# Optimization experiments

Measured on AMD Instinct MI355X. Metric: run time of the kernel, lower is better.

## Reference

```python
import jax, jax.numpy as jnp
import numpy as np

BM = 64; BN = 64          # block_m, block_n
NKM = BM // 4; NKN = BN // 4   # tokens sampled per block (16)
# topk_newtype bands: cumulative-pooled-attention fraction -> granularity value (0 = skip block)
RATIO_BANDS = [(1, 0.05), (2, 0.15), (4, 0.25), (8, 0.5)]


def setup_inputs() -> dict:
    key = jax.random.key(0)
    kq, kk, kv, ki, kj = jax.random.split(key, 5)
    B, H, L, D = 1, 8, 4096, 64
    q = jax.random.normal(kq, (B, H, L, D), jnp.float32)
    k = jax.random.normal(kk, (B, H, L, D), jnp.float32)
    v = jax.random.normal(kv, (B, H, L, D), jnp.float32)
    # distinct in-block sample positions, shared across blocks per (B,H)
    # (mirrors torch.topk(torch.rand(B,H,1,block), sample_num))
    sample_idx_q = jnp.argsort(jax.random.uniform(ki, (B, H, BM)), axis=-1)[..., :NKM].astype(jnp.int32)
    sample_idx_k = jnp.argsort(jax.random.uniform(kj, (B, H, BN)), axis=-1)[..., :NKN].astype(jnp.int32)
    return {"q": q, "k": k, "v": v, "sample_idx_q": sample_idx_q, "sample_idx_k": sample_idx_k}


def _sample_blocks(x, idx, bs, nk):
    # x: [B,H,L,D]; idx: [B,H,nk] in-block positions -> [B,H,nb*nk,D]
    B, H, L, D = x.shape
    nb = L // bs
    xb = x.reshape(B, H, nb, bs, D)
    gidx = jnp.broadcast_to(idx[:, :, None, :, None], (B, H, nb, nk, D))
    return jnp.take_along_axis(xb, gidx, axis=3).reshape(B, H, nb * nk, D)


def _block_mask(q, k, sample_idx_q, sample_idx_k):
    # pooled downsampled attention -> per-(q_block,k_block) keep mask (topk_newtype)
    B, H, L, D = q.shape
    qb, kb = L // BM, L // BN
    sq = _sample_blocks(q, sample_idx_q, BM, NKM)  # [B,H,qb*NKM,D]
    sk = _sample_blocks(k, sample_idx_k, BN, NKN)  # [B,H,kb*NKN,D]
    scores = jnp.einsum('bhqd,bhkd->bhqk', sq, sk) / jnp.sqrt(jnp.float32(D))
    attn = jax.nn.softmax(scores, axis=-1)
    # NKM x NKN sum-pooling == block-level pooled attention mass  [B,H,qb,kb]
    pooling = attn.reshape(B, H, qb, NKM, kb, NKN).sum(axis=(3, 5))
    # rank key-blocks per q-block row by pooled mass, band by cumulative fraction
    order = jnp.argsort(-pooling, axis=-1)
    sp = jnp.take_along_axis(pooling, order, axis=-1)
    cs = jnp.cumsum(sp, axis=-1)
    frac_before = (cs - sp) / cs[..., -1:]
    val = jnp.zeros_like(sp)
    for g, hi in RATIO_BANDS[::-1]:
        val = jnp.where(frac_before < hi, jnp.float32(g), val)
    rank = jnp.argsort(order, axis=-1)          # inverse permutation
    mask_vals = jnp.take_along_axis(val, rank, axis=-1)  # [B,H,qb,kb] in {0,1,2,4,8}
    return mask_vals > 0


def reference(q, k, v, sample_idx_q, sample_idx_k):
    B, H, L, D = q.shape
    attend = _block_mask(q, k, sample_idx_q, sample_idx_k)            # [B,H,qb,kb]
    attend_tok = jnp.repeat(jnp.repeat(attend, BM, axis=2), BN, axis=3)  # [B,H,L,L]
    scores = jnp.einsum('bhqd,bhkd->bhqk', q, k) / jnp.sqrt(jnp.float32(D))
    scores = jnp.where(attend_tok, scores, jnp.float32(-1e30))
    p = jax.nn.softmax(scores, axis=-1)
    return jnp.einsum('bhqk,bhkd->bhqd', p, v)
```

## Files before the change

kernel.cpp:

```cpp
#include <hip/hip_runtime.h>
#include <hip/hip_bf16.h>

#define H_ 8
#define L_ 4096
#define D_ 64
#define NB_ 64

typedef __attribute__((ext_vector_type(8))) short bf16x8;
typedef __attribute__((ext_vector_type(4))) float f32x4;

__device__ __forceinline__ unsigned short f2bf(float x) {
    unsigned u = __float_as_uint(x);
    u += 0x7fff + ((u >> 16) & 1);
    return (unsigned short)(u >> 16);
}
__device__ __forceinline__ float bf2f(unsigned short s) {
    return __uint_as_float(((unsigned)s) << 16);
}
__device__ __forceinline__ void gload_lds16(const unsigned short* g, unsigned short* l) {
    __builtin_amdgcn_global_load_lds(
        (const __attribute__((address_space(1))) unsigned int*)(const void*)g,
        (__attribute__((address_space(3))) unsigned int*)(void*)l,
        16, 0, 0);
}

__global__ __launch_bounds__(256) void prep_kernel(
    const float* __restrict__ q, const float* __restrict__ k, const float* __restrict__ v,
    const int* __restrict__ sidxk,
    unsigned short* __restrict__ qhi, unsigned short* __restrict__ qlo,
    unsigned short* __restrict__ khi,
    unsigned short* __restrict__ vth,
    unsigned short* __restrict__ skh, unsigned short* __restrict__ skl)
{
    const int h  = blockIdx.x >> 6;
    const int tb = blockIdx.x & 63;
    const int tid = threadIdx.x;
    __shared__ float vst[64][68];

    const size_t te = ((size_t)(h*64 + tb)) << 12;
    const float4* qg = (const float4*)(q + te);
    for (int i4 = tid; i4 < 1024; i4 += 256) {
        float4 t = qg[i4];
        ushort4 hi, lo;
        hi.x = f2bf(t.x); lo.x = f2bf(t.x - bf2f(hi.x));
        hi.y = f2bf(t.y); lo.y = f2bf(t.y - bf2f(hi.y));
        hi.z = f2bf(t.z); lo.z = f2bf(t.z - bf2f(hi.z));
        hi.w = f2bf(t.w); lo.w = f2bf(t.w - bf2f(hi.w));
        *(ushort4*)(qhi + te + i4*4) = hi;
        *(ushort4*)(qlo + te + i4*4) = lo;
    }
    const float4* kg = (const float4*)(k + te);
    for (int i4 = tid; i4 < 1024; i4 += 256) {
        float4 t = kg[i4];
        int r = i4 >> 4, c4 = i4 & 15;
        int sch = (c4 >> 1) ^ ((r >> 2) & 7);
        ushort4 hi;
        hi.x = f2bf(t.x); hi.y = f2bf(t.y); hi.z = f2bf(t.z); hi.w = f2bf(t.w);
        *(ushort4*)(khi + te + r*64 + sch*8 + (c4 & 1)*4) = hi;
    }
    {
        int t = tid >> 4, d4 = tid & 15;
        int srow = tb*64 + sidxk[h*16 + t];
        float4 x = *(const float4*)(k + ((size_t)h*L_ + srow)*D_ + d4*4);
        ushort4 hi, lo;
        hi.x = f2bf(x.x); lo.x = f2bf(x.x - bf2f(hi.x));
        hi.y = f2bf(x.y); lo.y = f2bf(x.y - bf2f(hi.y));
        hi.z = f2bf(x.z); lo.z = f2bf(x.z - bf2f(hi.z));
        hi.w = f2bf(x.w); lo.w = f2bf(x.w - bf2f(hi.w));
        int sch = (d4 >> 1) ^ (t & 7);
        size_t dst = ((size_t)h*1024 + tb*16 + t)*64 + sch*8 + (d4 & 1)*4;
        *(ushort4*)(skh + dst) = hi;
        *(ushort4*)(skl + dst) = lo;
    }
    const float4* vg = (const float4*)(v + te);
    for (int i4 = tid; i4 < 1024; i4 += 256) {
        float4 t = vg[i4];
        *(float4*)&vst[i4 >> 4][(i4 & 15)*4] = t;
    }
    __syncthreads();
    for (int u = tid; u < 512; u += 256) {
        int d = u >> 3, kc8 = u & 7;
        int sch = kc8 ^ (d & 7);
        ushort4 h0, h1;
        h0.x = f2bf(vst[kc8*8+0][d]); h0.y = f2bf(vst[kc8*8+1][d]);
        h0.z = f2bf(vst[kc8*8+2][d]); h0.w = f2bf(vst[kc8*8+3][d]);
        h1.x = f2bf(vst[kc8*8+4][d]); h1.y = f2bf(vst[kc8*8+5][d]);
        h1.z = f2bf(vst[kc8*8+6][d]); h1.w = f2bf(vst[kc8*8+7][d]);
        *(ushort4*)(vth + te + d*64 + sch*8 + 0) = h0;
        *(ushort4*)(vth + te + d*64 + sch*8 + 4) = h1;
    }
}

__global__ __launch_bounds__(256, 4) void mask_mfma(
    const unsigned short* __restrict__ qhi, const unsigned short* __restrict__ qlo,
    const unsigned short* __restrict__ skh, const unsigned short* __restrict__ skl,
    const int* __restrict__ sidxq,
    unsigned long long* __restrict__ maskbits)
{
    const int h    = blockIdx.x & 7;
    const int qb   = blockIdx.x >> 3;
    const int tid  = threadIdx.x;
    const int wave = tid >> 6;
    const int lane = tid & 63;
    const int l16  = lane & 15;
    const int quad = lane >> 4;

    __shared__ __align__(16) unsigned short ch[8192];
    __shared__ __align__(16) unsigned short cl[8192];
    __shared__ float E[16][64];
    __shared__ float Z[16];
    __shared__ float pooled[64];

    for (int e = tid; e < 16*64; e += 256) (&E[0][0])[e] = 0.f;

    const int iqr = sidxq[h*16 + l16];
    const size_t qo = (((size_t)(h*64 + qb)) << 12) + (size_t)iqr*64;
    bf16x8 qh[2], ql[2];
    qh[0] = *(const bf16x8*)(qhi + qo + quad*8);
    qh[1] = *(const bf16x8*)(qhi + qo + 32 + quad*8);
    ql[0] = *(const bf16x8*)(qlo + qo + quad*8);
    ql[1] = *(const bf16x8*)(qlo + qo + 32 + quad*8);
    __syncthreads();

    for (int cc = 0; cc < 8; ++cc) {
        const bf16x8* gh = (const bf16x8*)(skh + ((size_t)h*1024 + cc*128)*64);
        const bf16x8* gl = (const bf16x8*)(skl + ((size_t)h*1024 + cc*128)*64);
        for (int i = tid; i < 1024; i += 256) {
            ((bf16x8*)ch)[i] = gh[i];
            ((bf16x8*)cl)[i] = gl[i];
        }
        __syncthreads();

        #pragma unroll
        for (int tt = 0; tt < 2; ++tt) {
            const int kb = cc*8 + wave*2 + tt;
            const int nb = (wave*2 + tt)*16;
            f32x4 sacc = (f32x4){0.f, 0.f, 0.f, 0.f};
            #pragma unroll
            for (int kc = 0; kc < 2; ++kc) {
                const int off = (nb + l16)*64 + (((kc*4 + quad) ^ (l16 & 7))*8);
                bf16x8 kh = *(const bf16x8*)&ch[off];
                bf16x8 kl = *(const bf16x8*)&cl[off];
                sacc = __builtin_amdgcn_mfma_f32_16x16x32_bf16(qh[kc], kh, sacc, 0, 0, 0);
                sacc = __builtin_amdgcn_mfma_f32_16x16x32_bf16(qh[kc], kl, sacc, 0, 0, 0);
                sacc = __builtin_amdgcn_mfma_f32_16x16x32_bf16(ql[kc], kh, sacc, 0, 0, 0);
                sacc = __builtin_amdgcn_mfma_f32_16x16x32_bf16(ql[kc], kl, sacc, 0, 0, 0);
            }
            #pragma unroll
            for (int r = 0; r < 4; ++r) {
                float p = __expf(sacc[r] * 0.125f);
                p += __shfl_xor(p, 1);
                p += __shfl_xor(p, 2);
                p += __shfl_xor(p, 4);
                p += __shfl_xor(p, 8);
                if (l16 == 0) E[quad*4 + r][kb] = p;
            }
        }
        __syncthreads();
    }

    if (tid < 16) {
        float s = 0.f;
        #pragma unroll
        for (int kb = 0; kb < 64; ++kb) s += E[tid][kb];
        Z[tid] = s;
    }
    __syncthreads();
    if (tid < 64) {
        float s = 0.f;
        #pragma unroll
        for (int t = 0; t < 16; ++t) s += E[t][tid] / Z[t];
        pooled[tid] = s;
    }
    __syncthreads();
    if (tid < 64) {
        float pi = pooled[tid];
        float tot = 0.f, bef = 0.f;
        for (int j2 = 0; j2 < 64; ++j2) {
            float pj = pooled[j2];
            tot += pj;
            if (pj > pi || (pj == pi && j2 < tid)) bef += pj;
        }
        bool att = (bef / tot) < 0.5f;
        unsigned long long bits = __ballot(att);
        if (tid == 0) maskbits[h*64 + qb] = bits;
    }
}

__global__ __launch_bounds__(256, 2) void attn_fast(
    const unsigned short* __restrict__ qhi, const unsigned short* __restrict__ qlo,
    const unsigned short* __restrict__ khi,
    const unsigned short* __restrict__ vth,
    const unsigned long long* __restrict__ maskbits,
    float* __restrict__ out)
{
    const int h    = blockIdx.x & 7;
    const int qb   = blockIdx.x >> 3;
    const int tid  = threadIdx.x;
    const int wave = tid >> 6;
    const int lane = tid & 63;
    const int l16  = lane & 15;
    const int quad = lane >> 4;

    __shared__ __align__(16) unsigned short bufK[2][4096];
    __shared__ __align__(16) unsigned short bufVh[2][4096];
    __shared__ __align__(16) unsigned short ps[4][16][88];

    const size_t qoff = (((size_t)(h*64 + qb)) << 12) + (size_t)(wave*16 + l16)*64;
    bf16x8 qfh[2], qfl[2];
    qfh[0] = *(const bf16x8*)(qhi + qoff + quad*8);
    qfh[1] = *(const bf16x8*)(qhi + qoff + 32 + quad*8);
    qfl[0] = *(const bf16x8*)(qlo + qoff + quad*8);
    qfl[1] = *(const bf16x8*)(qlo + qoff + 32 + quad*8);

    const unsigned long long bm = maskbits[(h << 6) + qb];

    float lpart[4];
    f32x4 oacc[4];
    #pragma unroll
    for (int r = 0; r < 4; ++r) lpart[r] = 0.f;
    #pragma unroll
    for (int t = 0; t < 4; ++t) oacc[t] = (f32x4){0.f, 0.f, 0.f, 0.f};

    auto dma_stage = [&](int kb, int b) {
        const size_t tb = ((size_t)(h*64 + kb)) << 12;
        gload_lds16(khi + tb + tid*8,         &bufK [b][tid*8]);
        gload_lds16(khi + tb + (tid+256)*8,   &bufK [b][(tid+256)*8]);
        gload_lds16(vth + tb + tid*8,         &bufVh[b][tid*8]);
        gload_lds16(vth + tb + (tid+256)*8,   &bufVh[b][(tid+256)*8]);
    };

    auto compute = [&](int b) {
        f32x4 sacc[4];
        #pragma unroll
        for (int t = 0; t < 4; ++t) sacc[t] = (f32x4){0.f, 0.f, 0.f, 0.f};
        #pragma unroll
        for (int t = 0; t < 4; ++t) {
            #pragma unroll
            for (int kc = 0; kc < 2; ++kc) {
                bf16x8 kf = *(const bf16x8*)&bufK[b][(l16*4 + t)*64 + (((kc*4 + quad) ^ (l16 & 7))*8)];
                sacc[t] = __builtin_amdgcn_mfma_f32_16x16x32_bf16(qfh[kc], kf, sacc[t], 0, 0, 0);
                sacc[t] = __builtin_amdgcn_mfma_f32_16x16x32_bf16(qfl[kc], kf, sacc[t], 0, 0, 0);
            }
        }
        #pragma unroll
        for (int r = 0; r < 4; ++r) {
            float p0 = __expf(fmaf(sacc[0][r], 0.125f, -16.0f));
            float p1 = __expf(fmaf(sacc[1][r], 0.125f, -16.0f));
            float p2 = __expf(fmaf(sacc[2][r], 0.125f, -16.0f));
            float p3 = __expf(fmaf(sacc[3][r], 0.125f, -16.0f));
            __hip_bfloat162 a01 = __float22bfloat162_rn(make_float2(p0, p1));
            __hip_bfloat162 a23 = __float22bfloat162_rn(make_float2(p2, p3));
            unsigned u01 = *(unsigned*)&a01;
            unsigned u23 = *(unsigned*)&a23;
            uint2 w; w.x = u01; w.y = u23;
            *(uint2*)&ps[wave][quad*4 + r][l16*4] = w;
            lpart[r] += (bf2f((unsigned short)(u01 & 0xffffu)) + bf2f((unsigned short)(u01 >> 16)))
                      + (bf2f((unsigned short)(u23 & 0xffffu)) + bf2f((unsigned short)(u23 >> 16)));
        }
        bf16x8 pf[2];
        #pragma unroll
        for (int kc = 0; kc < 2; ++kc)
            pf[kc] = *(const bf16x8*)&ps[wave][l16][kc*32 + quad*8];
        #pragma unroll
        for (int t = 0; t < 4; ++t) {
            #pragma unroll
            for (int kc = 0; kc < 2; ++kc) {
                bf16x8 vh = *(const bf16x8*)&bufVh[b][(t*16 + l16)*64 + (((kc*4 + quad) ^ (l16 & 7))*8)];
                oacc[t] = __builtin_amdgcn_mfma_f32_16x16x32_bf16(pf[kc], vh, oacc[t], 0, 0, 0);
            }
        }
    };

    unsigned long long rem = bm;
    int cur = 0;
    {
        int kb0 = (int)__builtin_ctzll(rem); rem &= rem - 1;
        dma_stage(kb0, 0);
    }
    for (;;) {
        __syncthreads();
        int nxt = -1;
        if (rem) { nxt = (int)__builtin_ctzll(rem); rem &= rem - 1; dma_stage(nxt, cur ^ 1); }
        compute(cur);
        if (nxt < 0) break;
        cur ^= 1;
    }

    #pragma unroll
    for (int off = 1; off < 16; off <<= 1)
        #pragma unroll
        for (int r = 0; r < 4; ++r)
            lpart[r] += __shfl_xor(lpart[r], off);

    float* og = out + ((size_t)h*L_ + (size_t)qb*64)*D_ + (size_t)(wave*16 + quad*4)*D_;
    #pragma unroll
    for (int r = 0; r < 4; ++r) {
        float inv = 1.f / lpart[r];
        #pragma unroll
        for (int t = 0; t < 4; ++t)
            og[(size_t)r*D_ + t*16 + l16] = oacc[t][r] * inv;
    }
}

__global__ __launch_bounds__(256, 4) void mask_kernel4(
    const float* __restrict__ q, const float* __restrict__ k,
    const int* __restrict__ sidxq, const int* __restrict__ sidxk,
    unsigned long long* __restrict__ maskbits)
{
    const int h   = blockIdx.x >> 6;
    const int qb  = blockIdx.x & 63;
    const int tid = threadIdx.x;
    const int rg  = tid >> 5;
    const int cg  = tid & 31;

    __shared__ float sq[16][68];
    __shared__ float skc[128][68];
    __shared__ float E[16][64];
    __shared__ float Z[16];
    __shared__ float pooled[64];
    __shared__ int iq[16], ik[16];

    if (tid < 16) { iq[tid] = sidxq[h*16 + tid]; ik[tid] = sidxk[h*16 + tid]; }
    for (int e = tid; e < 16*64; e += 256) (&E[0][0])[e] = 0.f;
    __syncthreads();
    {
        int j = tid >> 4, d4 = tid & 15;
        int grow = h*L_ + qb*64 + iq[j];
        *(float4*)&sq[j][d4*4] = *(const float4*)(q + (size_t)grow*D_ + d4*4);
    }
    for (int cc = 0; cc < 8; ++cc) {
        for (int i = tid; i < 2048; i += 256) {
            int col = i >> 4, d4 = i & 15;
            int colg = cc*128 + col;
            int grow = h*L_ + (colg >> 4)*64 + ik[colg & 15];
            *(float4*)&skc[col][d4*4] = *(const float4*)(k + (size_t)grow*D_ + d4*4);
        }
        __syncthreads();
        float acc[2][4] = {{0.f,0.f,0.f,0.f},{0.f,0.f,0.f,0.f}};
        #pragma unroll 4
        for (int d4 = 0; d4 < 16; ++d4) {
            float4 qv0 = *(const float4*)&sq[rg*2 + 0][d4*4];
            float4 qv1 = *(const float4*)&sq[rg*2 + 1][d4*4];
            #pragma unroll
            for (int j = 0; j < 4; ++j) {
                float4 kv = *(const float4*)&skc[cg + 32*j][d4*4];
                acc[0][j] += qv0.x*kv.x + qv0.y*kv.y + qv0.z*kv.z + qv0.w*kv.w;
                acc[1][j] += qv1.x*kv.x + qv1.y*kv.y + qv1.z*kv.z + qv1.w*kv.w;
            }
        }
        #pragma unroll
        for (int j = 0; j < 4; ++j) {
            int kb = cc*8 + (cg >> 4) + 2*j;
            #pragma unroll
            for (int i = 0; i < 2; ++i) {
                float p = __expf(acc[i][j] * 0.125f);
                p += __shfl_xor(p, 1);
                p += __shfl_xor(p, 2);
                p += __shfl_xor(p, 4);
                p += __shfl_xor(p, 8);
                if ((cg & 15) == 0) E[rg*2 + i][kb] += p;
            }
        }
        __syncthreads();
    }
    if (tid < 16) {
        float s = 0.f;
        #pragma unroll
        for (int kb = 0; kb < 64; ++kb) s += E[tid][kb];
        Z[tid] = s;
    }
    __syncthreads();
    if (tid < 64) {
        float s = 0.f;
        #pragma unroll
        for (int t = 0; t < 16; ++t) s += E[t][tid] / Z[t];
        pooled[tid] = s;
    }
    __syncthreads();
    if (tid < 64) {
        float pi = pooled[tid];
        float tot = 0.f, bef = 0.f;
        for (int j2 = 0; j2 < 64; ++j2) {
            float pj = pooled[j2];
            tot += pj;
            if (pj > pi || (pj == pi && j2 < tid)) bef += pj;
        }
        bool att = (bef / tot) < 0.5f;
        unsigned long long bits = __ballot(att);
        if (tid == 0) maskbits[h*64 + qb] = bits;
    }
}

__global__ __launch_bounds__(256, 3) void attn_v3(
    const float* __restrict__ q, const float* __restrict__ k, const float* __restrict__ v,
    const unsigned long long* __restrict__ maskbits, float* __restrict__ out)
{
    const int h = blockIdx.x >> 6, qb = blockIdx.x & 63;
    const int tid = threadIdx.x, wave = tid >> 6, lane = tid & 63;
    const int l16 = lane & 15, quad = lane >> 4;
    __shared__ __align__(16) unsigned short ks_hi[64][72];
    __shared__ __align__(16) unsigned short ks_lo[64][72];
    __shared__ __align__(16) unsigned short vt_hi[64][72];
    __shared__ __align__(16) unsigned short vt_lo[64][72];
    __shared__ __align__(16) unsigned short ps[4][16][72];

    const float4* qg = (const float4*)(q + ((size_t)h*L_ + (size_t)qb*64)*D_);
    for (int i4 = tid; i4 < 1024; i4 += 256) {
        float4 t = qg[i4];
        int r = i4 >> 4, c = (i4 & 15) << 2;
        ushort4 hi, lo;
        hi.x = f2bf(t.x); lo.x = f2bf(t.x - bf2f(hi.x));
        hi.y = f2bf(t.y); lo.y = f2bf(t.y - bf2f(hi.y));
        hi.z = f2bf(t.z); lo.z = f2bf(t.z - bf2f(hi.z));
        hi.w = f2bf(t.w); lo.w = f2bf(t.w - bf2f(hi.w));
        *(ushort4*)&ks_hi[r][c] = hi;
        *(ushort4*)&ks_lo[r][c] = lo;
    }
    const unsigned long long bm = maskbits[(h << 6) + qb];
    __syncthreads();
    bf16x8 qhi2[2], qlo2[2];
    #pragma unroll
    for (int kc = 0; kc < 2; ++kc) {
        qhi2[kc] = *(const bf16x8*)&ks_hi[wave*16 + l16][kc*32 + quad*8];
        qlo2[kc] = *(const bf16x8*)&ks_lo[wave*16 + l16][kc*32 + quad*8];
    }
    __syncthreads();
    float m_i[4], l_i[4];
    f32x4 oacc[4];
    #pragma unroll
    for (int r = 0; r < 4; ++r) { m_i[r] = -1e30f; l_i[r] = 0.f; }
    #pragma unroll
    for (int t = 0; t < 4; ++t) oacc[t] = (f32x4){0.f, 0.f, 0.f, 0.f};
    for (int kb = 0; kb < 64; ++kb) {
        if (!((bm >> kb) & 1ull)) continue;
        const float4* kg = (const float4*)(k + ((size_t)h*L_ + (size_t)kb*64)*D_);
        const float*  vg = v + ((size_t)h*L_ + (size_t)kb*64)*D_;
        for (int i4 = tid; i4 < 1024; i4 += 256) {
            float4 t = kg[i4];
            int r = i4 >> 4, c = (i4 & 15) << 2;
            ushort4 hi, lo;
            hi.x = f2bf(t.x); lo.x = f2bf(t.x - bf2f(hi.x));
            hi.y = f2bf(t.y); lo.y = f2bf(t.y - bf2f(hi.y));
            hi.z = f2bf(t.z); lo.z = f2bf(t.z - bf2f(hi.z));
            hi.w = f2bf(t.w); lo.w = f2bf(t.w - bf2f(hi.w));
            *(ushort4*)&ks_hi[r][c] = hi;
            *(ushort4*)&ks_lo[r][c] = lo;
        }
        for (int tsk = tid; tsk < 512; tsk += 256) {
            int rp = tsk >> 4;
            int c  = (tsk & 15) << 2;
            float4 a0 = *(const float4*)(vg + (size_t)(2*rp)*D_ + c);
            float4 a1 = *(const float4*)(vg + (size_t)(2*rp+1)*D_ + c);
            #pragma unroll
            for (int j = 0; j < 4; ++j) {
                float x0 = (j==0)?a0.x:(j==1)?a0.y:(j==2)?a0.z:a0.w;
                float x1 = (j==0)?a1.x:(j==1)?a1.y:(j==2)?a1.z:a1.w;
                unsigned short h0 = f2bf(x0), h1b = f2bf(x1);
                *(unsigned*)&vt_hi[c+j][2*rp] = (unsigned)h0 | ((unsigned)h1b << 16);
                unsigned short lo0 = f2bf(x0 - bf2f(h0)), lo1 = f2bf(x1 - bf2f(h1b));
                *(unsigned*)&vt_lo[c+j][2*rp] = (unsigned)lo0 | ((unsigned)lo1 << 16);
            }
        }
        __syncthreads();
        f32x4 sacc[4];
        #pragma unroll
        for (int t = 0; t < 4; ++t) sacc[t] = (f32x4){0.f, 0.f, 0.f, 0.f};
        #pragma unroll
        for (int t = 0; t < 4; ++t) {
            #pragma unroll
            for (int kc = 0; kc < 2; ++kc) {
                bf16x8 khi2 = *(const bf16x8*)&ks_hi[t*16 + l16][kc*32 + quad*8];
                bf16x8 klo2 = *(const bf16x8*)&ks_lo[t*16 + l16][kc*32 + quad*8];
                sacc[t] = __builtin_amdgcn_mfma_f32_16x16x32_bf16(qhi2[kc], khi2, sacc[t], 0, 0, 0);
                sacc[t] = __builtin_amdgcn_mfma_f32_16x16x32_bf16(qhi2[kc], klo2, sacc[t], 0, 0, 0);
                sacc[t] = __builtin_amdgcn_mfma_f32_16x16x32_bf16(qlo2[kc], khi2, sacc[t], 0, 0, 0);
            }
        }
        #pragma unroll
        for (int t = 0; t < 4; ++t) sacc[t] *= 0.125f;
        float rowmax[4];
        #pragma unroll
        for (int r = 0; r < 4; ++r)
            rowmax[r] = fmaxf(fmaxf(sacc[0][r], sacc[1][r]), fmaxf(sacc[2][r], sacc[3][r]));
        #pragma unroll
        for (int off = 1; off < 16; off <<= 1)
            #pragma unroll
            for (int r = 0; r < 4; ++r)
                rowmax[r] = fmaxf(rowmax[r], __shfl_xor(rowmax[r], off));
        float al[4], rs[4];
        #pragma unroll
        for (int r = 0; r < 4; ++r) {
            float mnew = fmaxf(m_i[r], rowmax[r]);
            al[r] = __expf(m_i[r] - mnew);
            m_i[r] = mnew;
            float acc = 0.f;
            #pragma unroll
            for (int t = 0; t < 4; ++t) {
                float p = __expf(sacc[t][r] - mnew);
                unsigned short pb = f2bf(p);
                ps[wave][quad*4 + r][t*16 + l16] = pb;
                acc += bf2f(pb);
            }
            rs[r] = acc;
        }
        #pragma unroll
        for (int off = 1; off < 16; off <<= 1)
            #pragma unroll
            for (int r = 0; r < 4; ++r)
                rs[r] += __shfl_xor(rs[r], off);
        #pragma unroll
        for (int r = 0; r < 4; ++r) l_i[r] = l_i[r] * al[r] + rs[r];
        #pragma unroll
        for (int t = 0; t < 4; ++t)
            #pragma unroll
            for (int r = 0; r < 4; ++r) oacc[t][r] *= al[r];
        bf16x8 pf[2];
        #pragma unroll
        for (int kc = 0; kc < 2; ++kc)
            pf[kc] = *(const bf16x8*)&ps[wave][l16][kc*32 + quad*8];
        #pragma unroll
        for (int t = 0; t < 4; ++t) {
            #pragma unroll
            for (int kc = 0; kc < 2; ++kc) {
                bf16x8 vhif = *(const bf16x8*)&vt_hi[t*16 + l16][kc*32 + quad*8];
                bf16x8 vlof = *(const bf16x8*)&vt_lo[t*16 + l16][kc*32 + quad*8];
                oacc[t] = __builtin_amdgcn_mfma_f32_16x16x32_bf16(pf[kc], vhif, oacc[t], 0, 0, 0);
                oacc[t] = __builtin_amdgcn_mfma_f32_16x16x32_bf16(pf[kc], vlof, oacc[t], 0, 0, 0);
            }
        }
        __syncthreads();
    }
    float* og = out + ((size_t)h*L_ + (size_t)qb*64)*D_ + (size_t)(wave*16 + quad*4)*D_;
    #pragma unroll
    for (int r = 0; r < 4; ++r) {
        float inv = 1.f / l_i[r];
        #pragma unroll
        for (int t = 0; t < 4; ++t)
            og[(size_t)r*D_ + t*16 + l16] = oacc[t][r] * inv;
    }
}

extern "C" void kernel_launch(void* const* d_in, const int* in_sizes, int n_in,
                              void* d_out, int out_size, void* d_ws, size_t ws_size,
                              hipStream_t stream) {
    const float* q = (const float*)d_in[0];
    const float* k = (const float*)d_in[1];
    const float* v = (const float*)d_in[2];
    const int* siq = (const int*)d_in[3];
    const int* sik = (const int*)d_in[4];
    float* out = (float*)d_out;

    char* ws = (char*)d_ws;
    unsigned long long* mask = (unsigned long long*)ws;
    const size_t TEN = (size_t)H_*L_*D_;
    const size_t SKN = (size_t)H_*1024*64;
    unsigned short* qhi = (unsigned short*)(ws + 4096);
    unsigned short* qlo = qhi + TEN;
    unsigned short* khi = qlo + TEN;
    unsigned short* vth = khi + TEN;
    unsigned short* skh = vth + TEN;
    unsigned short* skl = skh + SKN;
    const size_t need = 4096 + (4*TEN + 2*SKN)*sizeof(unsigned short);

    if (ws_size >= need) {
        prep_kernel<<<dim3(H_*NB_), dim3(256), 0, stream>>>(q, k, v, sik, qhi, qlo, khi, vth, skh, skl);
        mask_mfma<<<dim3(H_*NB_), dim3(256), 0, stream>>>(qhi, qlo, skh, skl, siq, mask);
        attn_fast<<<dim3(H_*NB_), dim3(256), 0, stream>>>(qhi, qlo, khi, vth, mask, out);
    } else {
        mask_kernel4<<<dim3(H_*NB_), dim3(256), 0, stream>>>(q, k, siq, sik, mask);
        attn_v3<<<dim3(H_*NB_), dim3(256), 0, stream>>>(q, k, v, mask, out);
    }
}
```

Baseline: 146.7 us.

## Triple-buffer K/V tiles with explicit vmcnt waits and MFMA priority boosts

The K/V LDS staging grows from two buffers to three, so two tiles are prefetched ahead and each iteration waits only for the oldest outstanding DMA (vmcnt(4)) instead of fully draining. The synchronisation becomes a raw s_barrier with a sched_barrier, and the MFMA sections are wrapped in s_setprio to favour matrix work over other waves. LDS use grows by 16 KB per block, which may limit the intended two blocks per CU. Correctness depends on the hand-counted vmcnt values and on the write-after-read ordering of the ring buffer.

```diff
diff --git a/kernel.cpp b/kernel.cpp
--- a/kernel.cpp
+++ b/kernel.cpp
@@ -202,8 +202,8 @@
     const int l16  = lane & 15;
     const int quad = lane >> 4;
 
-    __shared__ __align__(16) unsigned short bufK[2][4096];
-    __shared__ __align__(16) unsigned short bufVh[2][4096];
+    __shared__ __align__(16) unsigned short bufK [3][4096];
+    __shared__ __align__(16) unsigned short bufVh[3][4096];
     __shared__ __align__(16) unsigned short ps[4][16][88];
 
     const size_t qoff = (((size_t)(h*64 + qb)) << 12) + (size_t)(wave*16 + l16)*64;
@@ -234,6 +234,7 @@
         f32x4 sacc[4];
         #pragma unroll
         for (int t = 0; t < 4; ++t) sacc[t] = (f32x4){0.f, 0.f, 0.f, 0.f};
+        __builtin_amdgcn_s_setprio(1);
         #pragma unroll
         for (int t = 0; t < 4; ++t) {
             #pragma unroll
@@ -243,6 +244,7 @@
                 sacc[t] = __builtin_amdgcn_mfma_f32_16x16x32_bf16(qfl[kc], kf, sacc[t], 0, 0, 0);
             }
         }
+        __builtin_amdgcn_s_setprio(0);
         #pragma unroll
         for (int r = 0; r < 4; ++r) {
             float p0 = __expf(fmaf(sacc[0][r], 0.125f, -16.0f));
@@ -262,6 +264,7 @@
         #pragma unroll
         for (int kc = 0; kc < 2; ++kc)
             pf[kc] = *(const bf16x8*)&ps[wave][l16][kc*32 + quad*8];
+        __builtin_amdgcn_s_setprio(1);
         #pragma unroll
         for (int t = 0; t < 4; ++t) {
             #pragma unroll
@@ -270,21 +273,36 @@
                 oacc[t] = __builtin_amdgcn_mfma_f32_16x16x32_bf16(pf[kc], vh, oacc[t], 0, 0, 0);
             }
         }
+        __builtin_amdgcn_s_setprio(0);
     };
 
     unsigned long long rem = bm;
-    int cur = 0;
+    int cur = 0, have_nxt = 0;
     {
         int kb0 = (int)__builtin_ctzll(rem); rem &= rem - 1;
         dma_stage(kb0, 0);
+        if (rem) {
+            int kb1 = (int)__builtin_ctzll(rem); rem &= rem - 1;
+            dma_stage(kb1, 1);
+            have_nxt = 1;
+        }
     }
     for (;;) {
-        __syncthreads();
-        int nxt = -1;
-        if (rem) { nxt = (int)__builtin_ctzll(rem); rem &= rem - 1; dma_stage(nxt, cur ^ 1); }
+        if (have_nxt) { asm volatile("s_waitcnt vmcnt(4)" ::: "memory"); }
+        else          { asm volatile("s_waitcnt vmcnt(0)" ::: "memory"); }
+        __builtin_amdgcn_sched_barrier(0);
+        __builtin_amdgcn_s_barrier();
+        int nxt2 = 0;
+        if (have_nxt && rem) {
+            int kb2 = (int)__builtin_ctzll(rem); rem &= rem - 1;
+            int b2 = cur + 2; if (b2 >= 3) b2 -= 3;
+            dma_stage(kb2, b2);
+            nxt2 = 1;
+        }
         compute(cur);
-        if (nxt < 0) break;
-        cur ^= 1;
+        if (!have_nxt) break;
+        have_nxt = nxt2;
+        cur = cur + 1; if (cur >= 3) cur = 0;
     }
 
     #pragma unroll
```

Result: faster. 143.8 us (-2.0%).

## Split attention key blocks across two workgroups and combine partial sums

Applied to the files above, without the earlier changes.

The attention kernel now launches two workgroups per (head, q-block), each taking alternating key blocks from the mask. The two write unnormalised partial outputs and row sums, and a new combine kernel adds and normalises them. The change aims to raise parallelism and occupancy on a 512-block grid with few active key blocks. It also splits the K and V staging so V has a single buffer with explicit waitcnt and barriers, and raises MFMA priority with setprio. In exchange it adds an extra kernel launch and a round trip of partial results through global memory.

```diff
diff --git a/kernel.cpp b/kernel.cpp
--- a/kernel.cpp
+++ b/kernel.cpp
@@ -187,15 +187,16 @@
     }
 }
 
-__global__ __launch_bounds__(256, 2) void attn_fast(
+__global__ __launch_bounds__(256, 4) void attn_split(
     const unsigned short* __restrict__ qhi, const unsigned short* __restrict__ qlo,
     const unsigned short* __restrict__ khi,
     const unsigned short* __restrict__ vth,
     const unsigned long long* __restrict__ maskbits,
-    float* __restrict__ out)
+    float* __restrict__ part_o, float* __restrict__ part_l)
 {
-    const int h    = blockIdx.x & 7;
-    const int qb   = blockIdx.x >> 3;
+    const int h     = blockIdx.x & 7;
+    const int qb    = (blockIdx.x >> 3) & 63;
+    const int split = blockIdx.x >> 9;
     const int tid  = threadIdx.x;
     const int wave = tid >> 6;
     const int lane = tid & 63;
@@ -203,7 +204,7 @@
     const int quad = lane >> 4;
 
     __shared__ __align__(16) unsigned short bufK[2][4096];
-    __shared__ __align__(16) unsigned short bufVh[2][4096];
+    __shared__ __align__(16) unsigned short bufV[4096];
     __shared__ __align__(16) unsigned short ps[4][16][88];
 
     const size_t qoff = (((size_t)(h*64 + qb)) << 12) + (size_t)(wave*16 + l16)*64;
@@ -213,7 +214,8 @@
     qfl[0] = *(const bf16x8*)(qlo + qoff + quad*8);
     qfl[1] = *(const bf16x8*)(qlo + qoff + 32 + quad*8);
 
-    const unsigned long long bm = maskbits[(h << 6) + qb];
+    unsigned long long rem = maskbits[(h << 6) + qb];
+    if (split && rem) rem &= rem - 1;
 
     float lpart[4];
     f32x4 oacc[4];
@@ -222,69 +224,83 @@
     #pragma unroll
     for (int t = 0; t < 4; ++t) oacc[t] = (f32x4){0.f, 0.f, 0.f, 0.f};
 
-    auto dma_stage = [&](int kb, int b) {
+    auto stage_K = [&](int kb, int b) {
         const size_t tb = ((size_t)(h*64 + kb)) << 12;
-        gload_lds16(khi + tb + tid*8,         &bufK [b][tid*8]);
-        gload_lds16(khi + tb + (tid+256)*8,   &bufK [b][(tid+256)*8]);
-        gload_lds16(vth + tb + tid*8,         &bufVh[b][tid*8]);
-        gload_lds16(vth + tb + (tid+256)*8,   &bufVh[b][(tid+256)*8]);
+        gload_lds16(khi + tb + tid*8,       &bufK[b][tid*8]);
+        gload_lds16(khi + tb + (tid+256)*8, &bufK[b][(tid+256)*8]);
     };
-
-    auto compute = [&](int b) {
-        f32x4 sacc[4];
-        #pragma unroll
-        for (int t = 0; t < 4; ++t) sacc[t] = (f32x4){0.f, 0.f, 0.f, 0.f};
-        #pragma unroll
-        for (int t = 0; t < 4; ++t) {
-            #pragma unroll
-            for (int kc = 0; kc < 2; ++kc) {
-                bf16x8 kf = *(const bf16x8*)&bufK[b][(l16*4 + t)*64 + (((kc*4 + quad) ^ (l16 & 7))*8)];
-                sacc[t] = __builtin_amdgcn_mfma_f32_16x16x32_bf16(qfh[kc], kf, sacc[t], 0, 0, 0);
-                sacc[t] = __builtin_amdgcn_mfma_f32_16x16x32_bf16(qfl[kc], kf, sacc[t], 0, 0, 0);
-            }
-        }
-        #pragma unroll
-        for (int r = 0; r < 4; ++r) {
-            float p0 = __expf(fmaf(sacc[0][r], 0.125f, -16.0f));
-            float p1 = __expf(fmaf(sacc[1][r], 0.125f, -16.0f));
-            float p2 = __expf(fmaf(sacc[2][r], 0.125f, -16.0f));
-            float p3 = __expf(fmaf(sacc[3][r], 0.125f, -16.0f));
-            __hip_bfloat162 a01 = __float22bfloat162_rn(make_float2(p0, p1));
-            __hip_bfloat162 a23 = __float22bfloat162_rn(make_float2(p2, p3));
-            unsigned u01 = *(unsigned*)&a01;
-            unsigned u23 = *(unsigned*)&a23;
-            uint2 w; w.x = u01; w.y = u23;
-            *(uint2*)&ps[wave][quad*4 + r][l16*4] = w;
-            lpart[r] += (bf2f((unsigned short)(u01 & 0xffffu)) + bf2f((unsigned short)(u01 >> 16)))
-                      + (bf2f((unsigned short)(u23 & 0xffffu)) + bf2f((unsigned short)(u23 >> 16)));
-        }
-        bf16x8 pf[2];
-        #pragma unroll
-        for (int kc = 0; kc < 2; ++kc)
-            pf[kc] = *(const bf16x8*)&ps[wave][l16][kc*32 + quad*8];
-        #pragma unroll
-        for (int t = 0; t < 4; ++t) {
-            #pragma unroll
-            for (int kc = 0; kc < 2; ++kc) {
-                bf16x8 vh = *(const bf16x8*)&bufVh[b][(t*16 + l16)*64 + (((kc*4 + quad) ^ (l16 & 7))*8)];
-                oacc[t] = __builtin_amdgcn_mfma_f32_16x16x32_bf16(pf[kc], vh, oacc[t], 0, 0, 0);
-            }
-        }
+    auto stage_V = [&](int kb) {
+        const size_t tb = ((size_t)(h*64 + kb)) << 12;
+        gload_lds16(vth + tb + tid*8,       &bufV[tid*8]);
+        gload_lds16(vth + tb + (tid+256)*8, &bufV[(tid+256)*8]);
     };
 
-    unsigned long long rem = bm;
-    int cur = 0;
-    {
-        int kb0 = (int)__builtin_ctzll(rem); rem &= rem - 1;
-        dma_stage(kb0, 0);
-    }
-    for (;;) {
-        __syncthreads();
-        int nxt = -1;
-        if (rem) { nxt = (int)__builtin_ctzll(rem); rem &= rem - 1; dma_stage(nxt, cur ^ 1); }
-        compute(cur);
-        if (nxt < 0) break;
-        cur ^= 1;
+    if (rem) {
+        int kb_cur = (int)__builtin_ctzll(rem);
+        rem &= rem - 1; if (rem) rem &= rem - 1;
+        stage_K(kb_cur, 0);
+        int cur = 0;
+        for (;;) {
+            asm volatile("s_waitcnt vmcnt(0)" ::: "memory");
+            __builtin_amdgcn_sched_barrier(0);
+            __builtin_amdgcn_s_barrier();
+            stage_V(kb_cur);
+            int kb_nxt = -1;
+            if (rem) {
+                kb_nxt = (int)__builtin_ctzll(rem);
+                rem &= rem - 1; if (rem) rem &= rem - 1;
+                stage_K(kb_nxt, cur ^ 1);
+            }
+            f32x4 sacc[4];
+            #pragma unroll
+            for (int t = 0; t < 4; ++t) sacc[t] = (f32x4){0.f, 0.f, 0.f, 0.f};
+            __builtin_amdgcn_s_setprio(1);
+            #pragma unroll
+            for (int t = 0; t < 4; ++t) {
+                #pragma unroll
+                for (int kc = 0; kc < 2; ++kc) {
+                    bf16x8 kf = *(const bf16x8*)&bufK[cur][(l16*4 + t)*64 + (((kc*4 + quad) ^ (l16 & 7))*8)];
+                    sacc[t] = __builtin_amdgcn_mfma_f32_16x16x32_bf16(qfh[kc], kf, sacc[t], 0, 0, 0);
+                    sacc[t] = __builtin_amdgcn_mfma_f32_16x16x32_bf16(qfl[kc], kf, sacc[t], 0, 0, 0);
+                }
+            }
+            __builtin_amdgcn_s_setprio(0);
+            #pragma unroll
+            for (int r = 0; r < 4; ++r) {
+                float p0 = __expf(fmaf(sacc[0][r], 0.125f, -16.0f));
+                float p1 = __expf(fmaf(sacc[1][r], 0.125f, -16.0f));
+                float p2 = __expf(fmaf(sacc[2][r], 0.125f, -16.0f));
+                float p3 = __expf(fmaf(sacc[3][r], 0.125f, -16.0f));
+                __hip_bfloat162 a01 = __float22bfloat162_rn(make_float2(p0, p1));
+                __hip_bfloat162 a23 = __float22bfloat162_rn(make_float2(p2, p3));
+                unsigned u01 = *(unsigned*)&a01;
+                unsigned u23 = *(unsigned*)&a23;
+                uint2 w; w.x = u01; w.y = u23;
+                *(uint2*)&ps[wave][quad*4 + r][l16*4] = w;
+                lpart[r] += (bf2f((unsigned short)(u01 & 0xffffu)) + bf2f((unsigned short)(u01 >> 16)))
+                          + (bf2f((unsigned short)(u23 & 0xffffu)) + bf2f((unsigned short)(u23 >> 16)));
+            }
+            if (kb_nxt >= 0) { asm volatile("s_waitcnt vmcnt(2)" ::: "memory"); }
+            else             { asm volatile("s_waitcnt vmcnt(0)" ::: "memory"); }
+            __builtin_amdgcn_sched_barrier(0);
+            __builtin_amdgcn_s_barrier();
+            bf16x8 pf[2];
+            #pragma unroll
+            for (int kc = 0; kc < 2; ++kc)
+                pf[kc] = *(const bf16x8*)&ps[wave][l16][kc*32 + quad*8];
+            __builtin_amdgcn_s_setprio(1);
+            #pragma unroll
+            for (int t = 0; t < 4; ++t) {
+                #pragma unroll
+                for (int kc = 0; kc < 2; ++kc) {
+                    bf16x8 vh = *(const bf16x8*)&bufV[(t*16 + l16)*64 + (((kc*4 + quad) ^ (l16 & 7))*8)];
+                    oacc[t] = __builtin_amdgcn_mfma_f32_16x16x32_bf16(pf[kc], vh, oacc[t], 0, 0, 0);
+                }
+            }
+            __builtin_amdgcn_s_setprio(0);
+            if (kb_nxt < 0) break;
+            kb_cur = kb_nxt; cur ^= 1;
+        }
     }
 
     #pragma unroll
@@ -293,13 +309,42 @@
         for (int r = 0; r < 4; ++r)
             lpart[r] += __shfl_xor(lpart[r], off);
 
-    float* og = out + ((size_t)h*L_ + (size_t)qb*64)*D_ + (size_t)(wave*16 + quad*4)*D_;
-    #pragma unroll
-    for (int r = 0; r < 4; ++r) {
-        float inv = 1.f / lpart[r];
+    const size_t blk = (size_t)split*512 + (size_t)(h*64 + qb);
+    float* po = part_o + (blk*64 + (size_t)(wave*16 + quad*4))*64;
+    #pragma unroll
+    for (int r = 0; r < 4; ++r)
         #pragma unroll
         for (int t = 0; t < 4; ++t)
-            og[(size_t)r*D_ + t*16 + l16] = oacc[t][r] * inv;
+            po[(size_t)r*64 + t*16 + l16] = oacc[t][r];
+    if (l16 == 0) {
+        #pragma unroll
+        for (int r = 0; r < 4; ++r)
+            part_l[blk*64 + wave*16 + quad*4 + r] = lpart[r];
+    }
+}
+
+__global__ __launch_bounds__(256) void combine_kernel(
+    const float* __restrict__ part_o, const float* __restrict__ part_l,
+    float* __restrict__ out)
+{
+    const int hq  = blockIdx.x;
+    const int tid = threadIdx.x;
+    const int row = tid >> 2;
+    const int d0  = (tid & 3) << 4;
+    const size_t S1o = (size_t)512*64*64;
+    const float l = part_l[(size_t)hq*64 + row] + part_l[(size_t)512*64 + hq*64 + row];
+    const float inv = 1.f / l;
+    const size_t base = ((size_t)hq*64 + row)*64 + d0;
+    #pragma unroll
+    for (int j = 0; j < 16; j += 4) {
+        float4 a = *(const float4*)(part_o + base + j);
+        float4 b = *(const float4*)(part_o + S1o + base + j);
+        float4 r;
+        r.x = (a.x + b.x) * inv;
+        r.y = (a.y + b.y) * inv;
+        r.z = (a.z + b.z) * inv;
+        r.w = (a.w + b.w) * inv;
+        *(float4*)(out + base + j) = r;
     }
 }
 
@@ -561,12 +606,16 @@
     unsigned short* vth = khi + TEN;
     unsigned short* skh = vth + TEN;
     unsigned short* skl = skh + SKN;
-    const size_t need = 4096 + (4*TEN + 2*SKN)*sizeof(unsigned short);
+    const size_t base_need = 4096 + (4*TEN + 2*SKN)*sizeof(unsigned short);
+    float* part_o = (float*)(ws + base_need);
+    float* part_l = part_o + (size_t)2*512*64*64;
+    const size_t need = base_need + ((size_t)2*512*64*64 + (size_t)2*512*64)*sizeof(float);
 
     if (ws_size >= need) {
         prep_kernel<<<dim3(H_*NB_), dim3(256), 0, stream>>>(q, k, v, sik, qhi, qlo, khi, vth, skh, skl);
         mask_mfma<<<dim3(H_*NB_), dim3(256), 0, stream>>>(qhi, qlo, skh, skl, siq, mask);
-        attn_fast<<<dim3(H_*NB_), dim3(256), 0, stream>>>(qhi, qlo, khi, vth, mask, out);
+        attn_split<<<dim3(H_*NB_*2), dim3(256), 0, stream>>>(qhi, qlo, khi, vth, mask, part_o, part_l);
+        combine_kernel<<<dim3(H_*NB_), dim3(256), 0, stream>>>(part_o, part_l, out);
     } else {
         mask_kernel4<<<dim3(H_*NB_), dim3(256), 0, stream>>>(q, k, siq, sik, mask);
         attn_v3<<<dim3(H_*NB_), dim3(256), 0, stream>>>(q, k, v, mask, out);
```

Result: no change. 148.6 us (+1.3%).

## Process key blocks in pairs with split K/V staging and explicit waitcnt pipelining

Applied to the files above, without the earlier changes.

The attention kernel now handles two selected key blocks per iteration. K tiles are double-buffered a step ahead, and V tiles are loaded separately, overlapping with the QK/softmax phase. Waits on outstanding loads use explicit vmcnt counts and raw barriers, MFMA sections are given higher scheduling priority, and exp is computed via exp2 with prescaled constants. This halves the number of barrier-bound iterations and hides V load latency, at the cost of more LDS (larger K buffer and P scratch) and tricky manual wait counts.

```diff
diff --git a/kernel.cpp b/kernel.cpp
--- a/kernel.cpp
+++ b/kernel.cpp
@@ -187,7 +187,7 @@
     }
 }
 
-__global__ __launch_bounds__(256, 2) void attn_fast(
+__global__ __launch_bounds__(256, 2) void attn_pair(
     const unsigned short* __restrict__ qhi, const unsigned short* __restrict__ qlo,
     const unsigned short* __restrict__ khi,
     const unsigned short* __restrict__ vth,
@@ -202,9 +202,9 @@
     const int l16  = lane & 15;
     const int quad = lane >> 4;
 
-    __shared__ __align__(16) unsigned short bufK[2][4096];
-    __shared__ __align__(16) unsigned short bufVh[2][4096];
-    __shared__ __align__(16) unsigned short ps[4][16][88];
+    __shared__ __align__(16) unsigned short bufK[2][2][4096];
+    __shared__ __align__(16) unsigned short bufV[2][4096];
+    __shared__ __align__(16) unsigned short ps[4][16][152];
 
     const size_t qoff = (((size_t)(h*64 + qb)) << 12) + (size_t)(wave*16 + l16)*64;
     bf16x8 qfh[2], qfl[2];
@@ -213,7 +213,7 @@
     qfl[0] = *(const bf16x8*)(qlo + qoff + quad*8);
     qfl[1] = *(const bf16x8*)(qlo + qoff + 32 + quad*8);
 
-    const unsigned long long bm = maskbits[(h << 6) + qb];
+    unsigned long long rem = maskbits[(h << 6) + qb];
 
     float lpart[4];
     f32x4 oacc[4];
@@ -222,69 +222,109 @@
     #pragma unroll
     for (int t = 0; t < 4; ++t) oacc[t] = (f32x4){0.f, 0.f, 0.f, 0.f};
 
-    auto dma_stage = [&](int kb, int b) {
+    auto stage_K1 = [&](int kb, int slot, int ta) {
         const size_t tb = ((size_t)(h*64 + kb)) << 12;
-        gload_lds16(khi + tb + tid*8,         &bufK [b][tid*8]);
-        gload_lds16(khi + tb + (tid+256)*8,   &bufK [b][(tid+256)*8]);
-        gload_lds16(vth + tb + tid*8,         &bufVh[b][tid*8]);
-        gload_lds16(vth + tb + (tid+256)*8,   &bufVh[b][(tid+256)*8]);
+        gload_lds16(khi + tb + tid*8,       &bufK[slot][ta][tid*8]);
+        gload_lds16(khi + tb + (tid+256)*8, &bufK[slot][ta][(tid+256)*8]);
     };
-
-    auto compute = [&](int b) {
+    auto stage_V1 = [&](int kb, int ta) {
+        const size_t tb = ((size_t)(h*64 + kb)) << 12;
+        gload_lds16(vth + tb + tid*8,       &bufV[ta][tid*8]);
+        gload_lds16(vth + tb + (tid+256)*8, &bufV[ta][(tid+256)*8]);
+    };
+
+    auto qk_sm = [&](int cur, int ta) {
         f32x4 sacc[4];
         #pragma unroll
         for (int t = 0; t < 4; ++t) sacc[t] = (f32x4){0.f, 0.f, 0.f, 0.f};
+        __builtin_amdgcn_s_setprio(1);
         #pragma unroll
         for (int t = 0; t < 4; ++t) {
             #pragma unroll
             for (int kc = 0; kc < 2; ++kc) {
-                bf16x8 kf = *(const bf16x8*)&bufK[b][(l16*4 + t)*64 + (((kc*4 + quad) ^ (l16 & 7))*8)];
+                bf16x8 kf = *(const bf16x8*)&bufK[cur][ta][(l16*4 + t)*64 + (((kc*4 + quad) ^ (l16 & 7))*8)];
                 sacc[t] = __builtin_amdgcn_mfma_f32_16x16x32_bf16(qfh[kc], kf, sacc[t], 0, 0, 0);
                 sacc[t] = __builtin_amdgcn_mfma_f32_16x16x32_bf16(qfl[kc], kf, sacc[t], 0, 0, 0);
             }
         }
+        __builtin_amdgcn_s_setprio(0);
         #pragma unroll
         for (int r = 0; r < 4; ++r) {
-            float p0 = __expf(fmaf(sacc[0][r], 0.125f, -16.0f));
-            float p1 = __expf(fmaf(sacc[1][r], 0.125f, -16.0f));
-            float p2 = __expf(fmaf(sacc[2][r], 0.125f, -16.0f));
-            float p3 = __expf(fmaf(sacc[3][r], 0.125f, -16.0f));
+            float p0 = __builtin_amdgcn_exp2f(fmaf(sacc[0][r], 0.18033688f, -23.083121f));
+            float p1 = __builtin_amdgcn_exp2f(fmaf(sacc[1][r], 0.18033688f, -23.083121f));
+            float p2 = __builtin_amdgcn_exp2f(fmaf(sacc[2][r], 0.18033688f, -23.083121f));
+            float p3 = __builtin_amdgcn_exp2f(fmaf(sacc[3][r], 0.18033688f, -23.083121f));
             __hip_bfloat162 a01 = __float22bfloat162_rn(make_float2(p0, p1));
             __hip_bfloat162 a23 = __float22bfloat162_rn(make_float2(p2, p3));
             unsigned u01 = *(unsigned*)&a01;
             unsigned u23 = *(unsigned*)&a23;
             uint2 w; w.x = u01; w.y = u23;
-            *(uint2*)&ps[wave][quad*4 + r][l16*4] = w;
+            *(uint2*)&ps[wave][quad*4 + r][ta*64 + l16*4] = w;
             lpart[r] += (bf2f((unsigned short)(u01 & 0xffffu)) + bf2f((unsigned short)(u01 >> 16)))
                       + (bf2f((unsigned short)(u23 & 0xffffu)) + bf2f((unsigned short)(u23 >> 16)));
         }
-        bf16x8 pf[2];
-        #pragma unroll
-        for (int kc = 0; kc < 2; ++kc)
-            pf[kc] = *(const bf16x8*)&ps[wave][l16][kc*32 + quad*8];
-        #pragma unroll
-        for (int t = 0; t < 4; ++t) {
-            #pragma unroll
-            for (int kc = 0; kc < 2; ++kc) {
-                bf16x8 vh = *(const bf16x8*)&bufVh[b][(t*16 + l16)*64 + (((kc*4 + quad) ^ (l16 & 7))*8)];
-                oacc[t] = __builtin_amdgcn_mfma_f32_16x16x32_bf16(pf[kc], vh, oacc[t], 0, 0, 0);
-            }
-        }
     };
 
-    unsigned long long rem = bm;
-    int cur = 0;
-    {
-        int kb0 = (int)__builtin_ctzll(rem); rem &= rem - 1;
-        dma_stage(kb0, 0);
-    }
-    for (;;) {
-        __syncthreads();
-        int nxt = -1;
-        if (rem) { nxt = (int)__builtin_ctzll(rem); rem &= rem - 1; dma_stage(nxt, cur ^ 1); }
-        compute(cur);
-        if (nxt < 0) break;
-        cur ^= 1;
+    if (rem) {
+        int ka = (int)__builtin_ctzll(rem); rem &= rem - 1;
+        int kb2 = -1;
+        if (rem) { kb2 = (int)__builtin_ctzll(rem); rem &= rem - 1; }
+        stage_K1(ka, 0, 0);
+        if (kb2 >= 0) stage_K1(kb2, 0, 1);
+        int cur = 0;
+        for (;;) {
+            asm volatile("s_waitcnt vmcnt(0)" ::: "memory");
+            __builtin_amdgcn_sched_barrier(0);
+            __builtin_amdgcn_s_barrier();
+            stage_V1(ka, 0);
+            if (kb2 >= 0) stage_V1(kb2, 1);
+            int na = -1, nb = -1;
+            if (rem) {
+                na = (int)__builtin_ctzll(rem); rem &= rem - 1;
+                if (rem) { nb = (int)__builtin_ctzll(rem); rem &= rem - 1; }
+                stage_K1(na, cur ^ 1, 0);
+                if (nb >= 0) stage_K1(nb, cur ^ 1, 1);
+            }
+            qk_sm(cur, 0);
+            if (kb2 >= 0) qk_sm(cur, 1);
+            if (na >= 0) {
+                if (nb >= 0) { asm volatile("s_waitcnt vmcnt(4)" ::: "memory"); }
+                else         { asm volatile("s_waitcnt vmcnt(2)" ::: "memory"); }
+            } else           { asm volatile("s_waitcnt vmcnt(0)" ::: "memory"); }
+            __builtin_amdgcn_sched_barrier(0);
+            __builtin_amdgcn_s_barrier();
+            bf16x8 pfa[2], pfb[2];
+            #pragma unroll
+            for (int kc = 0; kc < 2; ++kc)
+                pfa[kc] = *(const bf16x8*)&ps[wave][l16][kc*32 + quad*8];
+            if (kb2 >= 0) {
+                #pragma unroll
+                for (int kc = 0; kc < 2; ++kc)
+                    pfb[kc] = *(const bf16x8*)&ps[wave][l16][64 + kc*32 + quad*8];
+            }
+            __builtin_amdgcn_s_setprio(1);
+            #pragma unroll
+            for (int t = 0; t < 4; ++t) {
+                #pragma unroll
+                for (int kc = 0; kc < 2; ++kc) {
+                    bf16x8 vh = *(const bf16x8*)&bufV[0][(t*16 + l16)*64 + (((kc*4 + quad) ^ (l16 & 7))*8)];
+                    oacc[t] = __builtin_amdgcn_mfma_f32_16x16x32_bf16(pfa[kc], vh, oacc[t], 0, 0, 0);
+                }
+            }
+            if (kb2 >= 0) {
+                #pragma unroll
+                for (int t = 0; t < 4; ++t) {
+                    #pragma unroll
+                    for (int kc = 0; kc < 2; ++kc) {
+                        bf16x8 vh = *(const bf16x8*)&bufV[1][(t*16 + l16)*64 + (((kc*4 + quad) ^ (l16 & 7))*8)];
+                        oacc[t] = __builtin_amdgcn_mfma_f32_16x16x32_bf16(pfb[kc], vh, oacc[t], 0, 0, 0);
+                    }
+                }
+            }
+            __builtin_amdgcn_s_setprio(0);
+            if (na < 0) break;
+            ka = na; kb2 = nb; cur ^= 1;
+        }
     }
 
     #pragma unroll
@@ -566,7 +606,7 @@
     if (ws_size >= need) {
         prep_kernel<<<dim3(H_*NB_), dim3(256), 0, stream>>>(q, k, v, sik, qhi, qlo, khi, vth, skh, skl);
         mask_mfma<<<dim3(H_*NB_), dim3(256), 0, stream>>>(qhi, qlo, skh, skl, siq, mask);
-        attn_fast<<<dim3(H_*NB_), dim3(256), 0, stream>>>(qhi, qlo, khi, vth, mask, out);
+        attn_pair<<<dim3(H_*NB_), dim3(256), 0, stream>>>(qhi, qlo, khi, vth, mask, out);
     } else {
         mask_kernel4<<<dim3(H_*NB_), dim3(256), 0, stream>>>(q, k, siq, sik, mask);
         attn_v3<<<dim3(H_*NB_), dim3(256), 0, stream>>>(q, k, v, mask, out);
```

Measured after the change: 142.8 us. 1.03x faster.
